# Kernel tuning notes

Hardware: AMD Instinct MI355X
Metric: run time of the kernel (lower is better)

Reference implementation:

```python
import jax, jax.numpy as jnp
import numpy as np


def setup_inputs() -> dict:
    key = jax.random.key(0)
    k1, k2, k3 = jax.random.split(key, 3)
    B, A, P, Cm, S, C, G = 2, 512, 8, 6, 4, 256, 8
    # per-scale (H, W) for each of the 6 cameras (same pyramid per camera)
    shapes = np.array([[64, 176], [32, 88], [16, 44], [8, 22]], np.int32)  # [S,2]
    spatial_shape = jnp.asarray(np.tile(shapes[None], (Cm, 1, 1)))  # [Cm,S,2]
    sizes = shapes[:, 0] * shapes[:, 1]  # rows per scale
    starts = np.concatenate([[0], np.cumsum(np.tile(sizes, Cm))])[:-1].reshape(Cm, S).astype(np.int32)
    N = int(sizes.sum() * Cm)  # 89760 flattened feature rows
    mc_ms_feat = jax.random.normal(k1, (B, N, C), jnp.float32)
    sampling_location = jax.random.uniform(k2, (B, A, P, Cm, 2), jnp.float32)
    w = jax.random.uniform(k3, (B, A, P, Cm, S, G), jnp.float32)
    weights = w / jnp.sum(w, axis=(2, 3, 4), keepdims=True)  # normalized over pts/cams/scales
    return {
        "mc_ms_feat": mc_ms_feat,
        "spatial_shape": spatial_shape,
        "scale_start_index": jnp.asarray(starts),
        "sampling_location": sampling_location,
        "weights": weights,
    }


def reference(mc_ms_feat, spatial_shape, scale_start_index, sampling_location, weights):
    B, N, C = mc_ms_feat.shape
    _, A, P, Cm, _ = sampling_location.shape
    S = spatial_shape.shape[1]
    G = weights.shape[-1]
    Hi = spatial_shape[..., 0]  # [Cm,S] int32
    Wi = spatial_shape[..., 1]
    Hf = Hi.astype(mc_ms_feat.dtype)
    Wf = Wi.astype(mc_ms_feat.dtype)
    # pixel-space coords per (b,a,p,cam,scale); align_corners=False convention
    x = sampling_location[..., 0][..., None] * Wf - 0.5  # [B,A,P,Cm,S]
    y = sampling_location[..., 1][..., None] * Hf - 0.5
    x0 = jnp.floor(x)
    y0 = jnp.floor(y)
    x0i = x0.astype(jnp.int32)
    y0i = y0.astype(jnp.int32)
    wx1 = x - x0
    wy1 = y - y0
    batch_ix = jnp.arange(B)[:, None]

    def corner(ix, iy, cw):
        valid = (ix >= 0) & (ix < Wi) & (iy >= 0) & (iy < Hi)
        idx = scale_start_index + jnp.clip(iy, 0, Hi - 1) * Wi + jnp.clip(ix, 0, Wi - 1)
        f = mc_ms_feat[batch_ix, idx.reshape(B, -1)]  # [B, A*P*Cm*S, C]
        cw = jnp.where(valid, cw, 0.0).reshape(B, -1, 1)
        return f * cw

    val = (corner(x0i, y0i, (1.0 - wx1) * (1.0 - wy1))
           + corner(x0i + 1, y0i, wx1 * (1.0 - wy1))
           + corner(x0i, y0i + 1, (1.0 - wx1) * wy1)
           + corner(x0i + 1, y0i + 1, wx1 * wy1))
    # channel groups: C -> (G, D); weight each group, reduce pts/cams/scales
    val = val.reshape(B, A, P, Cm, S, G, C // G)
    out = jnp.einsum('bapcsgd,bapcsg->bagd', val, weights)
    return out.reshape(B, A, C)
```

## Files before the change

### kernel.cpp

```cpp
#include <hip/hip_runtime.h>

constexpr int B  = 2;
constexpr int A  = 512;
constexpr int P  = 8;
constexpr int CM = 6;
constexpr int SC = 4;
constexpr int C  = 256;
constexpr int G  = 8;
constexpr int NCOMBO = P * CM * SC;
constexpr int NFEAT  = 89760;
constexpr int COMBOS_PER_WAVE = NCOMBO / 4;
constexpr int NGRP = COMBOS_PER_WAVE / 2;

__global__ __launch_bounds__(256, 4)
void deform_agg_kernel(const float* __restrict__ feat,
                       const int*   __restrict__ spatial,
                       const int*   __restrict__ scale_start,
                       const float* __restrict__ samp_loc,
                       const float* __restrict__ weights,
                       float*       __restrict__ out) {
  __shared__ int    s_idx[NCOMBO][4];
  __shared__ float  s_cw[NCOMBO][4];
  __shared__ float  s_wg[NCOMBO * G];
  __shared__ float4 s_red[4][64];

  const int tid = threadIdx.x;
  const int ba  = blockIdx.x;
  const int b   = ba >> 9;

  if (tid < NCOMBO) {
    const int p   = tid / (CM * SC);
    const int cam = (tid / SC) % CM;
    const int s   = tid & (SC - 1);
    const float* lp = samp_loc + ((size_t)(ba * P + p) * CM + cam) * 2;
    const float lx = lp[0];
    const float ly = lp[1];
    const int H  = spatial[(cam * SC + s) * 2 + 0];
    const int W  = spatial[(cam * SC + s) * 2 + 1];
    const int st = scale_start[cam * SC + s];

    const float x = lx * (float)W - 0.5f;
    const float y = ly * (float)H - 0.5f;
    const float x0f = floorf(x), y0f = floorf(y);
    const int   ix0 = (int)x0f,  iy0 = (int)y0f;
    const float wx1 = x - x0f,   wy1 = y - y0f;
    const float wx[2] = {1.f - wx1, wx1};
    const float wy[2] = {1.f - wy1, wy1};
    const int   ix[2] = {ix0, ix0 + 1};
    const int   iy[2] = {iy0, iy0 + 1};
#pragma unroll
    for (int cyi = 0; cyi < 2; ++cyi) {
#pragma unroll
      for (int cxi = 0; cxi < 2; ++cxi) {
        const int k  = cyi * 2 + cxi;
        const int cx = ix[cxi], cy = iy[cyi];
        const bool valid = (cx >= 0) && (cx < W) && (cy >= 0) && (cy < H);
        const int ccx = min(max(cx, 0), W - 1);
        const int ccy = min(max(cy, 0), H - 1);
        s_idx[tid][k] = (st + ccy * W + ccx) * (C / 4);
        s_cw[tid][k]  = valid ? wx[cxi] * wy[cyi] : 0.f;
      }
    }
  }
  {
    const float* wbase = weights + (size_t)ba * NCOMBO * G;
    for (int i = tid; i < NCOMBO * G; i += 256) s_wg[i] = wbase[i];
  }
  __syncthreads();

  const int wid  = tid >> 6;
  const int lane = tid & 63;
  const int g    = lane >> 3;
  const float4* fb = (const float4*)(feat + (size_t)b * NFEAT * C);

  float4 acc = {0.f, 0.f, 0.f, 0.f};
  const int c0 = wid * COMBOS_PER_WAVE;

  auto load_grp = [&](int grp, float4* f, float* cw) {
#pragma unroll
    for (int j = 0; j < 2; ++j) {
      const int c = c0 + grp * 2 + j;
      const float w = s_wg[c * G + g];
#pragma unroll
      for (int k = 0; k < 4; ++k) {
        cw[j * 4 + k] = s_cw[c][k] * w;
        f[j * 4 + k]  = fb[s_idx[c][k] + lane];
      }
    }
  };
  auto consume = [&](const float4* f, const float* cw) {
#pragma unroll
    for (int j = 0; j < 8; ++j) {
      acc.x = fmaf(f[j].x, cw[j], acc.x);
      acc.y = fmaf(f[j].y, cw[j], acc.y);
      acc.z = fmaf(f[j].z, cw[j], acc.z);
      acc.w = fmaf(f[j].w, cw[j], acc.w);
    }
  };

  float4 fA[8], fB[8];
  float  cwA[8], cwB[8];
  load_grp(0, fA, cwA);
#pragma unroll
  for (int it = 0; it < NGRP - 1; ++it) {
    if ((it & 1) == 0) {
      load_grp(it + 1, fB, cwB);
      consume(fA, cwA);
    } else {
      load_grp(it + 1, fA, cwA);
      consume(fB, cwB);
    }
  }
  consume(fB, cwB);

  s_red[wid][lane] = acc;
  __syncthreads();

  if (wid == 0) {
    const float4 r0 = s_red[0][lane];
    const float4 r1 = s_red[1][lane];
    const float4 r2 = s_red[2][lane];
    const float4 r3 = s_red[3][lane];
    float4 t;
    t.x = (r0.x + r1.x) + (r2.x + r3.x);
    t.y = (r0.y + r1.y) + (r2.y + r3.y);
    t.z = (r0.z + r1.z) + (r2.z + r3.z);
    t.w = (r0.w + r1.w) + (r2.w + r3.w);
    ((float4*)out)[(size_t)ba * (C / 4) + lane] = t;
  }
}

extern "C" void kernel_launch(void* const* d_in, const int* in_sizes, int n_in,
                              void* d_out, int out_size, void* d_ws, size_t ws_size,
                              hipStream_t stream) {
  const float* feat        = (const float*)d_in[0];
  const int*   spatial     = (const int*)d_in[1];
  const int*   scale_start = (const int*)d_in[2];
  const float* samp_loc    = (const float*)d_in[3];
  const float* weights     = (const float*)d_in[4];
  float*       out         = (float*)d_out;

  deform_agg_kernel<<<B * A, 256, 0, stream>>>(feat, spatial, scale_start,
                                               samp_loc, weights, out);
}
```

Before: 281.6 us.

## Convert features to fp16 in workspace before bilinear gather-aggregate

Adds a pre-pass kernel that converts the fp32 feature map into fp16 stored in the workspace, and the aggregation kernel then gathers half-precision values and converts them to float before accumulating. This halves the bytes moved per random gather. The conversion pass reads the whole feature tensor (about 184 MB) and writes it back at half size on every call, which adds a full streaming pass. The fp16 rounding also reduces accuracy.

```diff
diff --git a/kernel.cpp b/kernel.cpp
--- a/kernel.cpp
+++ b/kernel.cpp
@@ -1,4 +1,5 @@
 #include <hip/hip_runtime.h>
+#include <hip/hip_fp16.h>
 
 constexpr int B  = 2;
 constexpr int A  = 512;
@@ -12,8 +13,25 @@
 constexpr int COMBOS_PER_WAVE = NCOMBO / 4;
 constexpr int NGRP = COMBOS_PER_WAVE / 2;
 
+__global__ __launch_bounds__(256)
+void convert_fp16_kernel(const float* __restrict__ in,
+                         uint2* __restrict__ out,
+                         int n4) {
+  const float4* in4 = (const float4*)in;
+  int i = blockIdx.x * 256 + threadIdx.x;
+  const int stride = gridDim.x * 256;
+  for (; i < n4; i += stride) {
+    const float4 v = in4[i];
+    union { __half2 h; unsigned u; } a, b;
+    a.h = __floats2half2_rn(v.x, v.y);
+    b.h = __floats2half2_rn(v.z, v.w);
+    uint2 q; q.x = a.u; q.y = b.u;
+    out[i] = q;
+  }
+}
+
 __global__ __launch_bounds__(256, 4)
-void deform_agg_kernel(const float* __restrict__ feat,
+void deform_agg_kernel(const uint2* __restrict__ feat16,
                        const int*   __restrict__ spatial,
                        const int*   __restrict__ scale_start,
                        const float* __restrict__ samp_loc,
@@ -71,12 +89,12 @@
   const int wid  = tid >> 6;
   const int lane = tid & 63;
   const int g    = lane >> 3;
-  const float4* fb = (const float4*)(feat + (size_t)b * NFEAT * C);
+  const uint2* fb = feat16 + (size_t)b * NFEAT * (C / 4);
 
   float4 acc = {0.f, 0.f, 0.f, 0.f};
   const int c0 = wid * COMBOS_PER_WAVE;
 
-  auto load_grp = [&](int grp, float4* f, float* cw) {
+  auto load_grp = [&](int grp, uint2* f, float* cw) {
 #pragma unroll
     for (int j = 0; j < 2; ++j) {
       const int c = c0 + grp * 2 + j;
@@ -88,18 +106,22 @@
       }
     }
   };
-  auto consume = [&](const float4* f, const float* cw) {
+  auto consume = [&](const uint2* f, const float* cw) {
 #pragma unroll
     for (int j = 0; j < 8; ++j) {
-      acc.x = fmaf(f[j].x, cw[j], acc.x);
-      acc.y = fmaf(f[j].y, cw[j], acc.y);
-      acc.z = fmaf(f[j].z, cw[j], acc.z);
-      acc.w = fmaf(f[j].w, cw[j], acc.w);
+      const __half2 h0 = *reinterpret_cast<const __half2*>(&f[j].x);
+      const __half2 h1 = *reinterpret_cast<const __half2*>(&f[j].y);
+      const float2 v01 = __half22float2(h0);
+      const float2 v23 = __half22float2(h1);
+      acc.x = fmaf(v01.x, cw[j], acc.x);
+      acc.y = fmaf(v01.y, cw[j], acc.y);
+      acc.z = fmaf(v23.x, cw[j], acc.z);
+      acc.w = fmaf(v23.y, cw[j], acc.w);
     }
   };
 
-  float4 fA[8], fB[8];
-  float  cwA[8], cwB[8];
+  uint2 fA[8], fB[8];
+  float cwA[8], cwB[8];
   load_grp(0, fA, cwA);
 #pragma unroll
   for (int it = 0; it < NGRP - 1; ++it) {
@@ -139,7 +161,10 @@
   const float* samp_loc    = (const float*)d_in[3];
   const float* weights     = (const float*)d_in[4];
   float*       out         = (float*)d_out;
+  uint2*       feat16      = (uint2*)d_ws;
 
-  deform_agg_kernel<<<B * A, 256, 0, stream>>>(feat, spatial, scale_start,
+  const int n4 = in_sizes[0] / 4;
+  convert_fp16_kernel<<<2048, 256, 0, stream>>>(feat, feat16, n4);
+  deform_agg_kernel<<<B * A, 256, 0, stream>>>(feat16, spatial, scale_start,
                                                samp_loc, weights, out);
 }
```

Result: slower. 310.6 us (+10.3%).
